# Kernel optimization log

Hardware: AMD Instinct MI355X
Metric: run time of the kernel (lower is better)

## Reference

```python
import jax, jax.numpy as jnp
import numpy as np

NUM_HEADS = 16

def _rope_tables(seq_len, dim, dtype):
    # LongLlamaRotaryEmbedding: inv_freq = 1/10000^(2i/d), emb = cat(freqs, freqs)
    inv_freq = 1.0 / (10000.0 ** (jnp.arange(0, dim, 2, dtype=jnp.float32) / dim))
    t = jnp.arange(seq_len, dtype=jnp.float32)
    freqs = t[:, None] * inv_freq[None, :]            # [S, D/2]
    emb = jnp.concatenate([freqs, freqs], axis=-1)    # [S, D]
    return jnp.cos(emb).astype(dtype), jnp.sin(emb).astype(dtype)

def _rotate_half(x):
    x1, x2 = jnp.split(x, 2, axis=-1)
    return jnp.concatenate([-x2, x1], axis=-1)

def _rotate_one(x, cos, sin, pos):
    # x: [B,H,S,D]; pos: [B,S] int -> gather-indexed RoPE
    c = cos[pos][:, None, :, :]  # [B,1,S,D]
    s = sin[pos][:, None, :, :]
    return x * c + _rotate_half(x) * s

def setup_inputs() -> dict:
    key = jax.random.key(0)
    B, S, HID = 1, 4096, 2048
    ks = jax.random.split(key, 5)
    hidden_states = jax.random.normal(ks[0], (B, S, HID), dtype=jnp.float32)
    # causal additive mask [B,1,S,S]: 0 where allowed, large negative above diagonal
    causal = jnp.tril(jnp.ones((S, S), dtype=bool))
    attention_mask = jnp.where(causal, 0.0, -1e9).astype(jnp.float32)[None, None]
    attention_mask = jnp.broadcast_to(attention_mask, (B, 1, S, S))
    position_ids = jnp.broadcast_to(jnp.arange(S, dtype=jnp.int64), (B, S))
    scale = 0.02
    Wq = jax.random.normal(ks[1], (HID, HID), dtype=jnp.float32) * scale
    Wk = jax.random.normal(ks[2], (HID, HID), dtype=jnp.float32) * scale
    Wv = jax.random.normal(ks[3], (HID, HID), dtype=jnp.float32) * scale
    Wo = jax.random.normal(ks[4], (HID, HID), dtype=jnp.float32) * scale
    return {"hidden_states": hidden_states, "attention_mask": attention_mask,
            "position_ids": position_ids, "Wq": Wq, "Wk": Wk, "Wv": Wv, "Wo": Wo}

def reference(hidden_states, attention_mask, position_ids, Wq, Wk, Wv, Wo):
    B, S, HID = hidden_states.shape
    H = NUM_HEADS
    D = HID // H
    # QKV projections (torch Linear: y = x @ W.T), shaped [B,H,S,D]
    q = (hidden_states @ Wq.T).reshape(B, S, H, D).transpose(0, 2, 1, 3)
    k = (hidden_states @ Wk.T).reshape(B, S, H, D).transpose(0, 2, 1, 3)
    v = (hidden_states @ Wv.T).reshape(B, S, H, D).transpose(0, 2, 1, 3)
    kv_seq_len = k.shape[-2]
    cos, sin = _rope_tables(kv_seq_len, D, hidden_states.dtype)
    # rel_pos_ids = position_ids - min over seq (gather-indexed RoPE)
    rel = position_ids - jnp.min(position_ids, axis=-1, keepdims=True)
    q = _rotate_one(q, cos, sin, rel[:, -S:])
    k = _rotate_one(k, cos, sin, rel)
    scores = jnp.einsum('bhqd,bhkd->bhqk', q, k) / jnp.asarray(np.sqrt(D), hidden_states.dtype)
    scores = scores + attention_mask  # additive mask broadcast over heads
    attn = jax.nn.softmax(scores, axis=-1)
    out = jnp.einsum('bhqk,bhkd->bhqd', attn, v)
    out = out.transpose(0, 2, 1, 3).reshape(B, S, HID)
    return out @ Wo.T
```

## Files before the change

### kernel.cpp

```cpp
#include <hip/hip_runtime.h>
#include <stdint.h>

typedef uint16_t u16;
typedef __bf16 bf16x8 __attribute__((ext_vector_type(8)));
typedef float f32x4 __attribute__((ext_vector_type(4)));
typedef uint32_t u32x4 __attribute__((ext_vector_type(4)));

__device__ __forceinline__ u16 f2bf(float f) {
    uint32_t u = __builtin_bit_cast(uint32_t, f);
    u += 0x7fffu + ((u >> 16) & 1u);
    return (u16)(u >> 16);
}
__device__ __forceinline__ float bf2f(u16 h) {
    uint32_t u = ((uint32_t)h) << 16;
    return __builtin_bit_cast(float, u);
}

__global__ __launch_bounds__(256) void cvt_f32_bf16(const float* __restrict__ in,
                                                    u16* __restrict__ out, int n4) {
    int i = blockIdx.x * 256 + threadIdx.x;
    if (i >= n4) return;
    float4 v = ((const float4*)in)[i];
    u16 o[4] = { f2bf(v.x), f2bf(v.y), f2bf(v.z), f2bf(v.w) };
    *(uint64_t*)(out + 4 * (size_t)i) = *(const uint64_t*)o;
}

__device__ __forceinline__ void gload16(const u16* g, u16* l) {
    __builtin_amdgcn_global_load_lds(
        (const __attribute__((address_space(1))) void*)g,
        (__attribute__((address_space(3))) void*)l, 16, 0, 0);
}

__global__ __launch_bounds__(512, 1) void gemm_qkv(const u16* __restrict__ A,
                                                   const u16* __restrict__ B,
                                                   u16* __restrict__ Cq,
                                                   int K) {
    __shared__ u16 As[2][16384];
    __shared__ u16 Bs[2][12288];
    const int tid  = threadIdx.x;
    const int wave = tid >> 6, lane = tid & 63;
    const int quad = lane >> 4, ln = lane & 15;
    const int wm = wave >> 2, wn = wave & 3;
    const int bm = blockIdx.x, bn = blockIdx.y;
    const int NT = K >> 6;
    const u16* Ab = A + (size_t)bm * 256 * K;
    const u16* Bb = B + (size_t)bn * 192 * K;
    const int lr  = lane >> 3;
    const int lc8 = ((lane & 7) ^ lr) * 8;
    const int sw  = ln & 7;
    const int cA0 = ((0 + quad) ^ sw) * 8;
    const int cA1 = ((4 + quad) ^ sw) * 8;

    f32x4 acc[8][3] = {};

    auto stage_a = [&](int t, int q) {
        int ch = q * 8 + wave;
        gload16(Ab + (size_t)(ch * 8 + lr) * K + t * 64 + lc8, &As[t & 1][ch * 512]);
    };
    auto stage_b = [&](int t, int q) {
        int ch = q * 8 + wave;
        gload16(Bb + (size_t)(ch * 8 + lr) * K + t * 64 + lc8, &Bs[t & 1][ch * 512]);
    };

    for (int q = 0; q < 4; q++) stage_a(0, q);
    for (int q = 0; q < 3; q++) stage_b(0, q);
    for (int q = 0; q < 4; q++) stage_a(1, q);
    asm volatile("s_waitcnt vmcnt(4)" ::: "memory");
    __builtin_amdgcn_s_barrier();

    for (int t = 0; t < NT; ++t) {
        const u16* Asb = As[t & 1];
        const u16* Bsb = Bs[t & 1];
        bf16x8 a0[8], a1[8], b0[3], b1[3];
#pragma unroll
        for (int i = 0; i < 8; i++)
            a0[i] = *(const bf16x8*)(Asb + (wm * 128 + i * 16 + ln) * 64 + cA0);
#pragma unroll
        for (int j = 0; j < 3; j++)
            b0[j] = *(const bf16x8*)(Bsb + (wn * 48 + j * 16 + ln) * 64 + cA0);
        if (t + 1 < NT) { stage_b(t + 1, 0); stage_b(t + 1, 1); }
        __builtin_amdgcn_s_barrier();
        asm volatile("s_waitcnt lgkmcnt(0)" ::: "memory");
        __builtin_amdgcn_s_setprio(1);
#pragma unroll
        for (int i = 0; i < 4; i++)
#pragma unroll
            for (int j = 0; j < 3; j++)
                acc[i][j] = __builtin_amdgcn_mfma_f32_16x16x32_bf16(a0[i], b0[j], acc[i][j], 0, 0, 0);
        __builtin_amdgcn_s_setprio(0);
        __builtin_amdgcn_s_barrier();
#pragma unroll
        for (int i = 0; i < 8; i++)
            a1[i] = *(const bf16x8*)(Asb + (wm * 128 + i * 16 + ln) * 64 + cA1);
#pragma unroll
        for (int j = 0; j < 3; j++)
            b1[j] = *(const bf16x8*)(Bsb + (wn * 48 + j * 16 + ln) * 64 + cA1);
        if (t + 1 < NT) stage_b(t + 1, 2);
        __builtin_amdgcn_s_barrier();
        asm volatile("s_waitcnt lgkmcnt(0)" ::: "memory");
        __builtin_amdgcn_s_setprio(1);
#pragma unroll
        for (int i = 4; i < 8; i++)
#pragma unroll
            for (int j = 0; j < 3; j++)
                acc[i][j] = __builtin_amdgcn_mfma_f32_16x16x32_bf16(a0[i], b0[j], acc[i][j], 0, 0, 0);
        __builtin_amdgcn_s_setprio(0);
        __builtin_amdgcn_s_barrier();
        if (t + 2 < NT) { stage_a(t + 2, 0); stage_a(t + 2, 1); }
        __builtin_amdgcn_s_barrier();
        __builtin_amdgcn_s_setprio(1);
#pragma unroll
        for (int i = 0; i < 4; i++)
#pragma unroll
            for (int j = 0; j < 3; j++)
                acc[i][j] = __builtin_amdgcn_mfma_f32_16x16x32_bf16(a1[i], b1[j], acc[i][j], 0, 0, 0);
        __builtin_amdgcn_s_setprio(0);
        __builtin_amdgcn_s_barrier();
        if (t + 2 < NT) { stage_a(t + 2, 2); stage_a(t + 2, 3); }
        __builtin_amdgcn_s_barrier();
        __builtin_amdgcn_s_setprio(1);
#pragma unroll
        for (int i = 4; i < 8; i++)
#pragma unroll
            for (int j = 0; j < 3; j++)
                acc[i][j] = __builtin_amdgcn_mfma_f32_16x16x32_bf16(a1[i], b1[j], acc[i][j], 0, 0, 0);
        __builtin_amdgcn_s_setprio(0);
        asm volatile("s_waitcnt vmcnt(4)" ::: "memory");
        __builtin_amdgcn_s_barrier();
    }
#pragma unroll
    for (int i = 0; i < 8; i++) {
        size_t row0 = (size_t)(bm * 256 + wm * 128 + i * 16 + quad * 4);
#pragma unroll
        for (int j = 0; j < 3; j++) {
            int n = bn * 192 + wn * 48 + j * 16 + ln;
            size_t off = ((size_t)(n >> 11) << 23) + (size_t)(n & 2047);
#pragma unroll
            for (int r = 0; r < 4; r++)
                Cq[off + (row0 + r) * 2048] = f2bf(acc[i][j][r]);
        }
    }
}

__global__ __launch_bounds__(256) void gemm_bt64(const u16* __restrict__ A,
                                                 const u16* __restrict__ B,
                                                 float* __restrict__ C,
                                                 int M, int N, int K) {
    __shared__ u16 As[64 * 32];
    __shared__ u16 Bs[128 * 32];
    const int tid  = threadIdx.x;
    const int wave = tid >> 6, lane = tid & 63;
    const int quad = lane >> 4, ln = lane & 15;
    const int bm = blockIdx.x, bn = blockIdx.y;
    const int wm = (wave & 1) * 32, wn = (wave >> 1) * 64;
    const u16* Ab = A + (size_t)bm * 64 * K;
    const u16* Bb = B + (size_t)bn * 128 * K;
    const int pa = wave * 64 + lane, ra = pa >> 2, ga = (pa & 3) * 8;

    f32x4 acc[2][4] = {};
    for (int k0 = 0; k0 < K; k0 += 32) {
        gload16(Ab + (size_t)ra * K + k0 + ga, As + wave * 512);
#pragma unroll
        for (int t = 0; t < 2; t++) {
            int p = (wave * 2 + t) * 64 + lane;
            int r = p >> 2, g = (p & 3) * 8;
            gload16(Bb + (size_t)r * K + k0 + g, Bs + (wave * 2 + t) * 512);
        }
        __syncthreads();
        bf16x8 a[2], b[4];
#pragma unroll
        for (int i = 0; i < 2; i++)
            a[i] = *(const bf16x8*)(As + (wm + i * 16 + ln) * 32 + quad * 8);
#pragma unroll
        for (int j = 0; j < 4; j++)
            b[j] = *(const bf16x8*)(Bs + (wn + j * 16 + ln) * 32 + quad * 8);
#pragma unroll
        for (int i = 0; i < 2; i++)
#pragma unroll
            for (int j = 0; j < 4; j++)
                acc[i][j] = __builtin_amdgcn_mfma_f32_16x16x32_bf16(a[i], b[j], acc[i][j], 0, 0, 0);
        __syncthreads();
    }
#pragma unroll
    for (int i = 0; i < 2; i++)
#pragma unroll
        for (int j = 0; j < 4; j++)
#pragma unroll
            for (int r = 0; r < 4; r++) {
                size_t row = (size_t)(bm * 64 + wm + i * 16 + quad * 4 + r);
                size_t col = (size_t)(bn * 128 + wn + j * 16 + ln);
                C[row * N + col] = acc[i][j][r];
            }
}

__global__ __launch_bounds__(256) void rope_scale(u16* __restrict__ Qb,
                                                  u16* __restrict__ Kb) {
    int idx = blockIdx.x * 256 + threadIdx.x;
    int s   = idx >> 11;
    int rem = idx & 2047;
    int mat = rem >> 10;
    int h   = (rem >> 6) & 15;
    int j   = rem & 63;
    u16* base = (mat ? Kb : Qb) + (size_t)s * 2048 + h * 128;
    float x1 = bf2f(base[j]);
    float x2 = bf2f(base[j + 64]);
    float invf = exp2f((float)(-j) * 0.2076205059304601f);
    float th = (float)s * invf;
    float sn, cs;
    sincosf(th, &sn, &cs);
    float o1 = x1 * cs - x2 * sn;
    float o2 = x2 * cs + x1 * sn;
    const float QS = 0.08838834764831845f * 1.4426950408889634f;
    if (mat == 0) { o1 *= QS; o2 *= QS; }
    base[j]      = f2bf(o1);
    base[j + 64] = f2bf(o2);
}

__global__ __launch_bounds__(256) void transpose_v(const u16* __restrict__ V,
                                                   u16* __restrict__ Vt) {
    const int h  = blockIdx.y;
    const int s0 = blockIdx.x * 64;
    const int tid = threadIdx.x;
    for (int c = tid; c < 1024; c += 256) {
        int d = c >> 3, sc = c & 7;
        u16 tmp[8];
#pragma unroll
        for (int j = 0; j < 8; j++)
            tmp[j] = V[(size_t)(s0 + sc * 8 + j) * 2048 + h * 128 + d];
        *(u32x4*)(Vt + ((size_t)h * 128 + d) * 4096 + s0 + sc * 8) = *(const u32x4*)tmp;
    }
}

__global__ __launch_bounds__(256, 3) void fattn(const u16* __restrict__ Qb,
                                                const u16* __restrict__ Kb,
                                                const u16* __restrict__ Vt,
                                                float* __restrict__ Oacc,
                                                float* __restrict__ Lacc) {
    __shared__ u16 Ks[2][32 * 128];
    __shared__ u16 Vs[2][128 * 32];
    __shared__ u16 Ps[128][40];
    const int tid  = threadIdx.x, wave = tid >> 6, lane = tid & 63;
    const int quad = lane >> 4, ln = lane & 15;
    const int h = blockIdx.x;
    const int y = blockIdx.y;
    int c, qt;
    if (y < 32)      { c = 0; qt = 31 - y; }
    else if (y < 56) { c = 1; qt = 63 - y; }
    else if (y < 72) { c = 2; qt = 87 - y; }
    else             { c = 3; qt = 103 - y; }
    const int q0 = qt * 128;
    const int nkt = min(32, 4 * qt + 4 - 32 * c);
    const int ktbase = 32 * c;

    const u16* Kp0 = Kb + h * 128;
    const u16* Vp0 = Vt + (size_t)h * 128 * 4096;

    bf16x8 aq[2][4];
    const u16* Qp = Qb + (size_t)q0 * 2048 + h * 128;
#pragma unroll
    for (int i = 0; i < 2; i++)
#pragma unroll
        for (int ks = 0; ks < 4; ks++)
            aq[i][ks] = *(const bf16x8*)(Qp + (size_t)(wave * 32 + i * 16 + ln) * 2048
                                         + ks * 32 + quad * 8);

    f32x4 o[2][8] = {};
    float lreg[2][4] = {};

    auto stage = [&](int kt, int b) {
        const u16* Kp = Kp0 + (size_t)(kt * 32) * 2048;
        const u16* Vp = Vp0 + kt * 32;
#pragma unroll
        for (int t = 0; t < 2; t++) {
            int p = (wave * 2 + t) * 64 + lane;
            int r = p >> 4, jc = (p & 15) ^ (r & 15);
            gload16(Kp + (size_t)r * 2048 + jc * 8, &Ks[b][(wave * 2 + t) * 512]);
        }
#pragma unroll
        for (int t = 0; t < 2; t++) {
            int p = (wave * 2 + t) * 64 + lane;
            int r = p >> 2, jc = (p & 3) ^ (r & 3);
            gload16(Vp + (size_t)r * 4096 + jc * 8, &Vs[b][(wave * 2 + t) * 512]);
        }
    };

    stage(ktbase, 0);
    for (int t = 0; t < nkt; t++) {
        __syncthreads();
        if (t + 1 < nkt) stage(ktbase + t + 1, (t + 1) & 1);
        const u16* Ksb = Ks[t & 1];
        const u16* Vsb = Vs[t & 1];

        f32x4 sc[2][2] = {};
#pragma unroll
        for (int ks = 0; ks < 4; ks++)
#pragma unroll
            for (int j = 0; j < 2; j++) {
                int r = j * 16 + ln;
                bf16x8 bk = *(const bf16x8*)(Ksb + (size_t)(r * 16 + ((ks * 4 + quad) ^ ln)) * 8);
                sc[0][j] = __builtin_amdgcn_mfma_f32_16x16x32_bf16(aq[0][ks], bk, sc[0][j], 0, 0, 0);
                sc[1][j] = __builtin_amdgcn_mfma_f32_16x16x32_bf16(aq[1][ks], bk, sc[1][j], 0, 0, 0);
            }
        const int kv0 = (ktbase + t) * 32;
        if (kv0 + 31 > q0 + wave * 32) {
#pragma unroll
            for (int j = 0; j < 2; j++) {
                int col = kv0 + j * 16 + ln;
#pragma unroll
                for (int i = 0; i < 2; i++)
#pragma unroll
                    for (int r = 0; r < 4; r++) {
                        int row = q0 + wave * 32 + i * 16 + quad * 4 + r;
                        if (col > row) sc[i][j][r] = -1e30f;
                    }
            }
        }
#pragma unroll
        for (int i = 0; i < 2; i++)
#pragma unroll
            for (int r = 0; r < 4; r++) {
                float p0 = __builtin_amdgcn_exp2f(sc[i][0][r]);
                float p1 = __builtin_amdgcn_exp2f(sc[i][1][r]);
                lreg[i][r] += p0 + p1;
                int row = wave * 32 + i * 16 + quad * 4 + r;
                Ps[row][ln]      = f2bf(p0);
                Ps[row][16 + ln] = f2bf(p1);
            }
        bf16x8 pa0 = *(const bf16x8*)&Ps[wave * 32 + ln][quad * 8];
        bf16x8 pa1 = *(const bf16x8*)&Ps[wave * 32 + 16 + ln][quad * 8];
#pragma unroll
        for (int n = 0; n < 8; n++) {
            int rv = n * 16 + ln;
            bf16x8 vb = *(const bf16x8*)(Vsb + (size_t)(rv * 4 + (quad ^ (ln & 3))) * 8);
            o[0][n] = __builtin_amdgcn_mfma_f32_16x16x32_bf16(pa0, vb, o[0][n], 0, 0, 0);
            o[1][n] = __builtin_amdgcn_mfma_f32_16x16x32_bf16(pa1, vb, o[1][n], 0, 0, 0);
        }
    }
    float* Op = Oacc + (size_t)(q0 + wave * 32) * 2048 + h * 128;
#pragma unroll
    for (int i = 0; i < 2; i++)
#pragma unroll
        for (int r = 0; r < 4; r++) {
            float l = lreg[i][r];
            l += __shfl_xor(l, 1);
            l += __shfl_xor(l, 2);
            l += __shfl_xor(l, 4);
            l += __shfl_xor(l, 8);
            int row = i * 16 + quad * 4 + r;
            if (ln == 0)
                unsafeAtomicAdd(&Lacc[(size_t)(q0 + wave * 32 + row) * 16 + h], l);
#pragma unroll
            for (int n = 0; n < 8; n++)
                unsafeAtomicAdd(&Op[(size_t)row * 2048 + n * 16 + ln], o[i][n][r]);
        }
}

__global__ __launch_bounds__(256) void attn_norm(const float* __restrict__ Oacc,
                                                 const float* __restrict__ Lacc,
                                                 u16* __restrict__ attn) {
    int i = blockIdx.x * 256 + threadIdx.x;
    int s  = i >> 9;
    int c4 = (i & 511) * 4;
    int h  = c4 >> 7;
    float inv = 1.0f / Lacc[(size_t)s * 16 + h];
    float4 v = ((const float4*)(Oacc + (size_t)s * 2048))[i & 511];
    u16 o[4] = { f2bf(v.x * inv), f2bf(v.y * inv), f2bf(v.z * inv), f2bf(v.w * inv) };
    *(uint64_t*)(attn + (size_t)s * 2048 + c4) = *(const uint64_t*)o;
}

extern "C" void kernel_launch(void* const* d_in, const int* in_sizes, int n_in,
                              void* d_out, int out_size, void* d_ws, size_t ws_size,
                              hipStream_t stream) {
    const float* hs = (const float*)d_in[0];
    const float* Wq = (const float*)d_in[3];
    const float* Wk = (const float*)d_in[4];
    const float* Wv = (const float*)d_in[5];
    const float* Wo = (const float*)d_in[6];

    char* ws = (char*)d_ws;
    u16* Xb   = (u16*)ws;
    u16* Wob  = (u16*)(ws + (size_t)16777216);
    u16* Qb   = (u16*)(ws + (size_t)25165824);
    u16* Kb   = (u16*)(ws + (size_t)41943040);
    u16* Vb   = (u16*)(ws + (size_t)58720256);
    u16* Wqkv = (u16*)(ws + (size_t)75497472);
    u16* Vtg  = (u16*)(ws + (size_t)100663296);
    float* Oacc = (float*)(ws + (size_t)58720256);
    float* Lacc = (float*)(ws + (size_t)92274688);
    u16* attn = Xb;

    cvt_f32_bf16<<<8192, 256, 0, stream>>>(hs, Xb, 2097152);
    cvt_f32_bf16<<<4096, 256, 0, stream>>>(Wq, Wqkv,            1048576);
    cvt_f32_bf16<<<4096, 256, 0, stream>>>(Wk, Wqkv + 4194304,  1048576);
    cvt_f32_bf16<<<4096, 256, 0, stream>>>(Wv, Wqkv + 8388608,  1048576);
    cvt_f32_bf16<<<4096, 256, 0, stream>>>(Wo, Wob,             1048576);

    gemm_qkv<<<dim3(16, 32), 512, 0, stream>>>(Xb, Wqkv, Qb, 2048);
    rope_scale<<<32768, 256, 0, stream>>>(Qb, Kb);
    transpose_v<<<dim3(64, 16), 256, 0, stream>>>(Vb, Vtg);
    hipMemsetAsync(Oacc, 0, 33816576, stream);
    fattn<<<dim3(16, 80), 256, 0, stream>>>(Qb, Kb, Vtg, Oacc, Lacc);
    attn_norm<<<8192, 256, 0, stream>>>(Oacc, Lacc, attn);
    gemm_bt64<<<dim3(64, 16), 256, 0, stream>>>(attn, Wob, (float*)d_out, 4096, 2048, 2048);
}
```

Baseline: 513.8 us.

## Rewrite output projection GEMM with larger pipelined tiles, fuse weight casts

The output-projection GEMM moves from a 64x128 tile with a 32-wide K step and full syncs to a 128x128 tile with a 64-wide K step. It uses double-buffered, XOR-swizzled LDS staging, interleaves async loads with MFMA phases, and raises wave priority around the MFMA blocks. The four weight-conversion launches are merged into one kernel, and the attention kernel gets setprio hints around its MFMA loops. The aim is better data reuse and overlap in the GEMM plus less launch overhead. In exchange the GEMM grid is smaller (512 blocks) and the barrier schedule is more intricate.

```diff
diff --git a/kernel.cpp b/kernel.cpp
--- a/kernel.cpp
+++ b/kernel.cpp
@@ -20,6 +20,22 @@
                                                     u16* __restrict__ out, int n4) {
     int i = blockIdx.x * 256 + threadIdx.x;
     if (i >= n4) return;
+    float4 v = ((const float4*)in)[i];
+    u16 o[4] = { f2bf(v.x), f2bf(v.y), f2bf(v.z), f2bf(v.w) };
+    *(uint64_t*)(out + 4 * (size_t)i) = *(const uint64_t*)o;
+}
+
+__global__ __launch_bounds__(256) void cvt_w4(const float* __restrict__ W0,
+                                              const float* __restrict__ W1,
+                                              const float* __restrict__ W2,
+                                              const float* __restrict__ W3,
+                                              u16* __restrict__ Wqkv,
+                                              u16* __restrict__ Wob) {
+    int b = blockIdx.x;
+    int w = b >> 12;
+    const float* in = (w == 0 ? W0 : w == 1 ? W1 : w == 2 ? W2 : W3);
+    u16* out = (w < 3 ? Wqkv + (size_t)w * 4194304 : Wob);
+    int i = (b & 4095) * 256 + threadIdx.x;
     float4 v = ((const float4*)in)[i];
     u16 o[4] = { f2bf(v.x), f2bf(v.y), f2bf(v.z), f2bf(v.w) };
     *(uint64_t*)(out + 4 * (size_t)i) = *(const uint64_t*)o;
@@ -142,54 +158,111 @@
     }
 }
 
-__global__ __launch_bounds__(256) void gemm_bt64(const u16* __restrict__ A,
+__global__ __launch_bounds__(256, 2) void gemm_o(const u16* __restrict__ A,
                                                  const u16* __restrict__ B,
                                                  float* __restrict__ C,
-                                                 int M, int N, int K) {
-    __shared__ u16 As[64 * 32];
-    __shared__ u16 Bs[128 * 32];
+                                                 int K) {
+    __shared__ u16 As[2][8192];
+    __shared__ u16 Bs[2][8192];
     const int tid  = threadIdx.x;
     const int wave = tid >> 6, lane = tid & 63;
     const int quad = lane >> 4, ln = lane & 15;
+    const int wm = (wave & 1) * 64, wn = (wave >> 1) * 64;
     const int bm = blockIdx.x, bn = blockIdx.y;
-    const int wm = (wave & 1) * 32, wn = (wave >> 1) * 64;
-    const u16* Ab = A + (size_t)bm * 64 * K;
+    const int NT = K >> 6;
+    const u16* Ab = A + (size_t)bm * 128 * K;
     const u16* Bb = B + (size_t)bn * 128 * K;
-    const int pa = wave * 64 + lane, ra = pa >> 2, ga = (pa & 3) * 8;
-
-    f32x4 acc[2][4] = {};
-    for (int k0 = 0; k0 < K; k0 += 32) {
-        gload16(Ab + (size_t)ra * K + k0 + ga, As + wave * 512);
-#pragma unroll
-        for (int t = 0; t < 2; t++) {
-            int p = (wave * 2 + t) * 64 + lane;
-            int r = p >> 2, g = (p & 3) * 8;
-            gload16(Bb + (size_t)r * K + k0 + g, Bs + (wave * 2 + t) * 512);
-        }
-        __syncthreads();
-        bf16x8 a[2], b[4];
+    const int lr  = lane >> 3;
+    const int lc8 = ((lane & 7) ^ lr) * 8;
+    const int sw  = ln & 7;
+    const int cA0 = ((0 + quad) ^ sw) * 8;
+    const int cA1 = ((4 + quad) ^ sw) * 8;
+
+    f32x4 acc[4][4] = {};
+
+    auto stage_a = [&](int t, int q) {
+        int ch = q * 4 + wave;
+        gload16(Ab + (size_t)(ch * 8 + lr) * K + t * 64 + lc8, &As[t & 1][ch * 512]);
+    };
+    auto stage_b = [&](int t, int q) {
+        int ch = q * 4 + wave;
+        gload16(Bb + (size_t)(ch * 8 + lr) * K + t * 64 + lc8, &Bs[t & 1][ch * 512]);
+    };
+
+    for (int q = 0; q < 4; q++) stage_a(0, q);
+    for (int q = 0; q < 4; q++) stage_b(0, q);
+    for (int q = 0; q < 4; q++) stage_a(1, q);
+    asm volatile("s_waitcnt vmcnt(4)" ::: "memory");
+    __builtin_amdgcn_s_barrier();
+
+    for (int t = 0; t < NT; ++t) {
+        const u16* Asb = As[t & 1];
+        const u16* Bsb = Bs[t & 1];
+        bf16x8 a0[4], a1[4], b0[4], b1[4];
+#pragma unroll
+        for (int i = 0; i < 4; i++) {
+            a0[i] = *(const bf16x8*)(Asb + (wm + i * 16 + ln) * 64 + cA0);
+            b0[i] = *(const bf16x8*)(Bsb + (wn + i * 16 + ln) * 64 + cA0);
+        }
+        if (t + 1 < NT) { stage_b(t + 1, 0); stage_b(t + 1, 1); }
+        __builtin_amdgcn_s_barrier();
+        asm volatile("s_waitcnt lgkmcnt(0)" ::: "memory");
+        __builtin_amdgcn_s_setprio(1);
 #pragma unroll
         for (int i = 0; i < 2; i++)
-            a[i] = *(const bf16x8*)(As + (wm + i * 16 + ln) * 32 + quad * 8);
+#pragma unroll
+            for (int j = 0; j < 4; j++)
+                acc[i][j] = __builtin_amdgcn_mfma_f32_16x16x32_bf16(a0[i], b0[j], acc[i][j], 0, 0, 0);
+        __builtin_amdgcn_s_setprio(0);
+        __builtin_amdgcn_s_barrier();
+#pragma unroll
+        for (int i = 0; i < 4; i++) {
+            a1[i] = *(const bf16x8*)(Asb + (wm + i * 16 + ln) * 64 + cA1);
+            b1[i] = *(const bf16x8*)(Bsb + (wn + i * 16 + ln) * 64 + cA1);
+        }
+        if (t + 1 < NT) { stage_b(t + 1, 2); stage_b(t + 1, 3); }
+        __builtin_amdgcn_s_barrier();
+        asm volatile("s_waitcnt lgkmcnt(0)" ::: "memory");
+        __builtin_amdgcn_s_setprio(1);
+#pragma unroll
+        for (int i = 2; i < 4; i++)
+#pragma unroll
+            for (int j = 0; j < 4; j++)
+                acc[i][j] = __builtin_amdgcn_mfma_f32_16x16x32_bf16(a0[i], b0[j], acc[i][j], 0, 0, 0);
+        __builtin_amdgcn_s_setprio(0);
+        __builtin_amdgcn_s_barrier();
+        if (t + 2 < NT) { stage_a(t + 2, 0); stage_a(t + 2, 1); }
+        __builtin_amdgcn_s_barrier();
+        __builtin_amdgcn_s_setprio(1);
+#pragma unroll
+        for (int i = 0; i < 2; i++)
+#pragma unroll
+            for (int j = 0; j < 4; j++)
+                acc[i][j] = __builtin_amdgcn_mfma_f32_16x16x32_bf16(a1[i], b1[j], acc[i][j], 0, 0, 0);
+        __builtin_amdgcn_s_setprio(0);
+        __builtin_amdgcn_s_barrier();
+        if (t + 2 < NT) { stage_a(t + 2, 2); stage_a(t + 2, 3); }
+        __builtin_amdgcn_s_barrier();
+        __builtin_amdgcn_s_setprio(1);
+#pragma unroll
+        for (int i = 2; i < 4; i++)
+#pragma unroll
+            for (int j = 0; j < 4; j++)
+                acc[i][j] = __builtin_amdgcn_mfma_f32_16x16x32_bf16(a1[i], b1[j], acc[i][j], 0, 0, 0);
+        __builtin_amdgcn_s_setprio(0);
+        if (t + 2 < NT) asm volatile("s_waitcnt vmcnt(4)" ::: "memory");
+        else            asm volatile("s_waitcnt vmcnt(0)" ::: "memory");
+        __builtin_amdgcn_s_barrier();
+    }
+#pragma unroll
+    for (int i = 0; i < 4; i++)
 #pragma unroll
         for (int j = 0; j < 4; j++)
-            b[j] = *(const bf16x8*)(Bs + (wn + j * 16 + ln) * 32 + quad * 8);
-#pragma unroll
-        for (int i = 0; i < 2; i++)
-#pragma unroll
-            for (int j = 0; j < 4; j++)
-                acc[i][j] = __builtin_amdgcn_mfma_f32_16x16x32_bf16(a[i], b[j], acc[i][j], 0, 0, 0);
-        __syncthreads();
-    }
-#pragma unroll
-    for (int i = 0; i < 2; i++)
-#pragma unroll
-        for (int j = 0; j < 4; j++)
 #pragma unroll
             for (int r = 0; r < 4; r++) {
-                size_t row = (size_t)(bm * 64 + wm + i * 16 + quad * 4 + r);
+                size_t row = (size_t)(bm * 128 + wm + i * 16 + quad * 4 + r);
                 size_t col = (size_t)(bn * 128 + wn + j * 16 + ln);
-                C[row * N + col] = acc[i][j][r];
+                C[row * 2048 + col] = acc[i][j][r];
             }
 }
 
@@ -292,6 +365,7 @@
         const u16* Vsb = Vs[t & 1];
 
         f32x4 sc[2][2] = {};
+        __builtin_amdgcn_s_setprio(1);
 #pragma unroll
         for (int ks = 0; ks < 4; ks++)
 #pragma unroll
@@ -301,6 +375,7 @@
                 sc[0][j] = __builtin_amdgcn_mfma_f32_16x16x32_bf16(aq[0][ks], bk, sc[0][j], 0, 0, 0);
                 sc[1][j] = __builtin_amdgcn_mfma_f32_16x16x32_bf16(aq[1][ks], bk, sc[1][j], 0, 0, 0);
             }
+        __builtin_amdgcn_s_setprio(0);
         const int kv0 = (ktbase + t) * 32;
         if (kv0 + 31 > q0 + wave * 32) {
 #pragma unroll
@@ -328,6 +403,7 @@
             }
         bf16x8 pa0 = *(const bf16x8*)&Ps[wave * 32 + ln][quad * 8];
         bf16x8 pa1 = *(const bf16x8*)&Ps[wave * 32 + 16 + ln][quad * 8];
+        __builtin_amdgcn_s_setprio(1);
 #pragma unroll
         for (int n = 0; n < 8; n++) {
             int rv = n * 16 + ln;
@@ -335,6 +411,7 @@
             o[0][n] = __builtin_amdgcn_mfma_f32_16x16x32_bf16(pa0, vb, o[0][n], 0, 0, 0);
             o[1][n] = __builtin_amdgcn_mfma_f32_16x16x32_bf16(pa1, vb, o[1][n], 0, 0, 0);
         }
+        __builtin_amdgcn_s_setprio(0);
     }
     float* Op = Oacc + (size_t)(q0 + wave * 32) * 2048 + h * 128;
 #pragma unroll
@@ -390,10 +467,7 @@
     u16* attn = Xb;
 
     cvt_f32_bf16<<<8192, 256, 0, stream>>>(hs, Xb, 2097152);
-    cvt_f32_bf16<<<4096, 256, 0, stream>>>(Wq, Wqkv,            1048576);
-    cvt_f32_bf16<<<4096, 256, 0, stream>>>(Wk, Wqkv + 4194304,  1048576);
-    cvt_f32_bf16<<<4096, 256, 0, stream>>>(Wv, Wqkv + 8388608,  1048576);
-    cvt_f32_bf16<<<4096, 256, 0, stream>>>(Wo, Wob,             1048576);
+    cvt_w4<<<16384, 256, 0, stream>>>(Wq, Wk, Wv, Wo, Wqkv, Wob);
 
     gemm_qkv<<<dim3(16, 32), 512, 0, stream>>>(Xb, Wqkv, Qb, 2048);
     rope_scale<<<32768, 256, 0, stream>>>(Qb, Kb);
@@ -401,5 +475,5 @@
     hipMemsetAsync(Oacc, 0, 33816576, stream);
     fattn<<<dim3(16, 80), 256, 0, stream>>>(Qb, Kb, Vtg, Oacc, Lacc);
     attn_norm<<<8192, 256, 0, stream>>>(Oacc, Lacc, attn);
-    gemm_bt64<<<dim3(64, 16), 256, 0, stream>>>(attn, Wob, (float*)d_out, 4096, 2048, 2048);
-}
+    gemm_o<<<dim3(32, 16), 256, 0, stream>>>(attn, Wob, (float*)d_out, 2048);
+}
```

After: 485.9 us. 5.4% less time.
